# Kernel optimization log

Measured on AMD Instinct MI355X. Metric: run time of the kernel, lower is better.

## Reference

```python
import jax, jax.numpy as jnp
import numpy as np

EMBED = 384; HEADS = 12; POINTS = 9; LAYERS = 2
KFG = 20; KBG = 50; NITER = 10
B = 4; H = 64; W = 64


def _layer_norm(x, g, b, eps=1e-5):
    m = x.mean(-1, keepdims=True)
    v = ((x - m) ** 2).mean(-1, keepdims=True)
    return (x - m) * jax.lax.rsqrt(v + eps) * g + b


def _sine_pos(pad, C):
    # pad [B,H,W], 1.0 = padded. SinePositionalEncoding(num_feats=C//2, normalize=True)
    nf = C // 2
    not_m = 1.0 - pad
    y = jnp.cumsum(not_m, axis=1)
    x = jnp.cumsum(not_m, axis=2)
    eps = 1e-6; sc = 2.0 * np.pi
    y = y / (y[:, -1:, :] + eps) * sc
    x = x / (x[:, :, -1:] + eps) * sc
    t = jnp.arange(nf, dtype=jnp.float32)
    dim_t = 10000.0 ** (2.0 * jnp.floor(t / 2.0) / nf)
    px = x[..., None] / dim_t
    py = y[..., None] / dim_t
    def inter(p):
        b_, h_, w_, _ = p.shape
        return jnp.stack((jnp.sin(p[..., 0::2]), jnp.cos(p[..., 1::2])), -1).reshape(b_, h_, w_, nf)
    pos = jnp.concatenate([inter(py), inter(px)], -1)  # [B,H,W,C]
    return pos.reshape(pad.shape[0], -1, C)


def _kmeans(x, w, K, n_iter):
    # masked Lloyd k-means. x [B,N,C], w [B,N] in {0,1} (1 = member of the group)
    Bq, N, C = x.shape
    score = w - (jnp.arange(N, dtype=x.dtype) / N) * 1e-3  # earliest in-group points first
    _, idx = jax.lax.top_k(score, K)
    centers = jnp.take_along_axis(x, idx[:, :, None], axis=1)  # [B,K,C]
    xsq = jnp.sum(x * x, -1)
    def body(i, c):
        d = xsq[:, :, None] - 2.0 * jnp.einsum('bnc,bkc->bnk', x, c) + jnp.sum(c * c, -1)[:, None, :]
        a = jax.nn.one_hot(jnp.argmin(d, -1), K, dtype=x.dtype) * w[:, :, None]
        num = jnp.einsum('bnk,bnc->bkc', a, x)
        den = jnp.sum(a, 1)[:, :, None]
        return jnp.where(den > 0, num / jnp.maximum(den, 1e-6), c)
    return jax.lax.fori_loop(0, n_iter, body, centers)


def _bilinear(value, loc, Hs, Ws):
    # value [B,heads,HW,hd]; loc [B,N,heads,P,2] normalized (x,y); zero padding outside
    Bq, nh, HW, hd = value.shape
    x = loc[..., 0] * Ws - 0.5
    y = loc[..., 1] * Hs - 0.5
    x0 = jnp.floor(x); y0 = jnp.floor(y)
    def tr(t):
        return jnp.transpose(t, (0, 2, 1, 3)).reshape(Bq, nh, -1)  # -> [B,heads,N*P]
    wx = tr(x - x0)[..., None]
    wy = tr(y - y0)[..., None]
    x0i = x0.astype(jnp.int32); y0i = y0.astype(jnp.int32)
    def gather(xi, yi):
        valid = (xi >= 0) & (xi < Ws) & (yi >= 0) & (yi < Hs)
        idx = jnp.clip(yi, 0, Hs - 1) * Ws + jnp.clip(xi, 0, Ws - 1)
        g = jnp.take_along_axis(value, tr(idx)[..., None], axis=2)  # [B,heads,N*P,hd]
        return g * tr(valid.astype(value.dtype))[..., None]
    v00 = gather(x0i, y0i)
    v01 = gather(x0i + 1, y0i)
    v10 = gather(x0i, y0i + 1)
    v11 = gather(x0i + 1, y0i + 1)
    out = v00 * (1 - wx) * (1 - wy) + v01 * wx * (1 - wy) + v10 * (1 - wx) * wy + v11 * wx * wy
    return out.reshape(Bq, nh, -1, POINTS, hd)  # [B,heads,N,P,hd]


def _forward(s_x, s_padding_mask, supp_mask, Wv, bv, Woff, boff, Wa, ba, Wout, bout,
             ln1_g, ln1_b, Wf1, Wf2, ln2_g, ln2_b):
    Bq, C, Hs, Ws = s_x.shape
    N = Hs * Ws
    hd = C // HEADS
    pad = (s_padding_mask[:, 0] == 255.0).astype(s_x.dtype)  # 1 = padded
    obj = (supp_mask[:, 0] == 1.0).astype(s_x.dtype)
    x = s_x.reshape(Bq, C, N).transpose(0, 2, 1)  # [B,N,C]
    padf = pad.reshape(Bq, N)
    objf = obj.reshape(Bq, N)
    # FG/BG k-means clustering of valid pixels (Cluster tool, n_iter=10)
    fg_c = _kmeans(x, objf * (1.0 - padf), KFG, NITER)
    bg_c = _kmeans(x, (1.0 - objf) * (1.0 - padf), KBG, NITER)
    pos = _sine_pos(pad, C)
    ry, rx = jnp.meshgrid(jnp.linspace(0.5, Hs - 0.5, Hs) / Hs,
                          jnp.linspace(0.5, Ws - 0.5, Ws) / Ws, indexing='ij')
    ref = jnp.stack([rx.reshape(-1), ry.reshape(-1)], -1)[None]  # [1,N,2] (x,y)
    wh = jnp.array([Ws, Hs], dtype=s_x.dtype)
    for l in range(LAYERS):
        q = x + pos
        v = (x * (1.0 - padf)[..., None]) @ Wv[l] + bv[l]
        v = v.reshape(Bq, N, HEADS, hd).transpose(0, 2, 1, 3)  # [B,heads,N,hd]
        off = (q @ Woff[l] + boff[l]).reshape(Bq, N, HEADS, POINTS, 2)
        aw = jax.nn.softmax((q @ Wa[l] + ba[l]).reshape(Bq, N, HEADS, POINTS), axis=-1)
        loc = ref[:, :, None, None, :] + off / wh
        samp = _bilinear(v, loc, Hs, Ws)  # [B,heads,N,P,hd]
        attn = jnp.einsum('bhnpd,bnhp->bnhd', samp, aw).reshape(Bq, N, C)
        x = _layer_norm(x + attn @ Wout[l] + bout[l], ln1_g[l], ln1_b[l])
        x = _layer_norm(x + jax.nn.relu(x @ Wf1[l]) @ Wf2[l], ln2_g[l], ln2_b[l])
    return jnp.concatenate([x, fg_c, bg_c], axis=1)  # [B, N+70, C]


def setup_inputs():
    key = jax.random.key(0)
    ks = jax.random.split(key, 12)
    dt = jnp.float32
    s = 0.02
    p = lambda k, shp: jax.random.normal(k, shp, dt) * s
    s_x = jax.random.normal(ks[0], (B, EMBED, H, W), dt)
    pad = jnp.zeros((B, 1, H, W), dt).at[:, :, :, W - 8:].set(255.0)  # right border padded
    supp_mask = (jax.random.uniform(ks[1], (B, 1, H, W)) < 0.15).astype(dt)
    return dict(
        s_x=s_x, s_padding_mask=pad, supp_mask=supp_mask,
        Wv=p(ks[2], (LAYERS, EMBED, EMBED)), bv=jnp.zeros((LAYERS, EMBED), dt),
        Woff=p(ks[3], (LAYERS, EMBED, HEADS * POINTS * 2)), boff=p(ks[4], (LAYERS, HEADS * POINTS * 2)),
        Wa=p(ks[5], (LAYERS, EMBED, HEADS * POINTS)), ba=jnp.zeros((LAYERS, HEADS * POINTS), dt),
        Wout=p(ks[6], (LAYERS, EMBED, EMBED)), bout=jnp.zeros((LAYERS, EMBED), dt),
        ln1_g=jnp.ones((LAYERS, EMBED), dt), ln1_b=jnp.zeros((LAYERS, EMBED), dt),
        Wf1=p(ks[7], (LAYERS, EMBED, 3 * EMBED)), Wf2=p(ks[8], (LAYERS, 3 * EMBED, EMBED)),
        ln2_g=jnp.ones((LAYERS, EMBED), dt), ln2_b=jnp.zeros((LAYERS, EMBED), dt))


def reference(s_x, s_padding_mask, supp_mask, Wv, bv, Woff, boff, Wa, ba, Wout, bout,
              ln1_g, ln1_b, Wf1, Wf2, ln2_g, ln2_b):
    return _forward(s_x, s_padding_mask, supp_mask, Wv, bv, Woff, boff, Wa, ba, Wout, bout,
                    ln1_g, ln1_b, Wf1, Wf2, ln2_g, ln2_b)
```

## Files before the change

kernel.cpp:

```cpp
#include <hip/hip_runtime.h>
#include <hip/hip_bf16.h>
#include <math.h>

#define NB 4
#define CE 384
#define NH 12
#define DH 32
#define NPTS 9
#define NLAYERS 2
#define KFG 20
#define KBG 50
#define NITER 10
#define HDIM 64
#define WDIM 64
#define NPIX 4096
#define BNTOT (NB * NPIX)
#define NROW (NPIX + KFG + KBG)
#define TWO_PI 6.283185307179586f

#define AS1 __attribute__((address_space(1)))
#define AS3 __attribute__((address_space(3)))

typedef __attribute__((ext_vector_type(8))) short short8;
typedef __attribute__((ext_vector_type(4))) float float4v;

static __device__ __forceinline__ unsigned short f2bf(float f) {
  __hip_bfloat16 h = __float2bfloat16(f);
  return *reinterpret_cast<unsigned short*>(&h);
}
static __device__ __forceinline__ float bf2f(unsigned short u) {
  unsigned x = ((unsigned)u) << 16;
  return __uint_as_float(x);
}

__device__ __forceinline__ float4 sample4(const float* __restrict__ vb, int xi, int yi, int c) {
  bool valid = (xi >= 0) & (xi < WDIM) & (yi >= 0) & (yi < HDIM);
  int xc = min(max(xi, 0), WDIM - 1), yc = min(max(yi, 0), HDIM - 1);
  float4 g = *(const float4*)(vb + (long)(yc * WDIM + xc) * CE + c);
  if (!valid) { g.x = 0.f; g.y = 0.f; g.z = 0.f; g.w = 0.f; }
  return g;
}

__global__ void k_masks(const float* __restrict__ pm, const float* __restrict__ sm,
                        float* padf, float* objf, float* notp, float* wfg, float* wbg) {
  int i = blockIdx.x * 256 + threadIdx.x;
  if (i >= NB * NPIX) return;
  float p  = (pm[i] == 255.0f) ? 1.f : 0.f;
  float o  = (sm[i] == 1.0f) ? 1.f : 0.f;
  float np_ = 1.f - p;
  padf[i] = p; objf[i] = o; notp[i] = np_;
  wfg[i] = o * np_;
  wbg[i] = (1.f - o) * np_;
}

__global__ __launch_bounds__(256) void k_transpose(const float* __restrict__ sx,
                                                   float* __restrict__ X) {
  __shared__ float tile[64][65];
  int nb = blockIdx.x * 64, cb = blockIdx.y * 64, b = blockIdx.z;
  int t = threadIdx.x;
  for (int idx = t; idx < 64 * 64; idx += 256) {
    int cc = idx >> 6, nn = idx & 63;
    tile[cc][nn] = sx[((long)b * CE + cb + cc) * NPIX + nb + nn];
  }
  __syncthreads();
  for (int idx = t; idx < 64 * 64; idx += 256) {
    int nn = idx >> 6, cc = idx & 63;
    X[((long)b * NPIX + nb + nn) * CE + cb + cc] = tile[cc][nn];
  }
}

__global__ void k_xsq(const float* __restrict__ X, double* __restrict__ xsq) {
  int row = blockIdx.x; int t = threadIdx.x;
  const float* xr = X + (long)row * CE;
  double s = 0.0;
  for (int i = t; i < CE; i += 64) { double v = (double)xr[i]; s += v * v; }
  #pragma unroll
  for (int o = 32; o > 0; o >>= 1) s += __shfl_down(s, o, 64);
  if (t == 0) xsq[row] = s;
}

__global__ __launch_bounds__(128) void k_cums(const float* __restrict__ padf,
                                              float* __restrict__ yvf,
                                              float* __restrict__ xvf,
                                              float* __restrict__ invdt) {
  __shared__ float pad_s[NPIX];
  int b = blockIdx.x; int t = threadIdx.x;
  for (int i = t; i < NPIX; i += 128) pad_s[i] = padf[b * NPIX + i];
  if (b == 0) {
    for (int c = t; c < CE; c += 128) {
      int tt = (c < 192) ? c : c - 192;
      invdt[c] = 1.0f / powf(10000.0f, (float)(2 * (tt / 2)) / 192.0f);
    }
  }
  __syncthreads();
  if (t < 64) {
    int w = t;
    float cum[64]; float tot = 0.f;
    for (int h = 0; h < 64; ++h) {
      float nm = 1.f - pad_s[h * WDIM + w];
      tot += nm; cum[h] = tot;
    }
    float sc = 1.f / (tot + 1e-6f);
    for (int h = 0; h < 64; ++h) yvf[b * NPIX + h * WDIM + w] = cum[h] * sc * TWO_PI;
  } else {
    int h = t - 64;
    float cum[64]; float tot = 0.f;
    for (int w = 0; w < 64; ++w) {
      float nm = 1.f - pad_s[h * WDIM + w];
      tot += nm; cum[w] = tot;
    }
    float sc = 1.f / (tot + 1e-6f);
    for (int w = 0; w < 64; ++w) xvf[b * NPIX + h * WDIM + w] = cum[w] * sc * TWO_PI;
  }
}

__global__ void k_kinit(const float* __restrict__ X, const float* __restrict__ wts,
                        float* __restrict__ cen, int K) {
  int b = blockIdx.x;
  __shared__ int idx[KBG];
  if (threadIdx.x == 0) {
    int cnt = 0;
    for (int n = 0; n < NPIX && cnt < K; ++n) if (wts[b * NPIX + n] > 0.f) idx[cnt++] = n;
    for (int n = 0; n < NPIX && cnt < K; ++n) if (!(wts[b * NPIX + n] > 0.f)) idx[cnt++] = n;
  }
  __syncthreads();
  for (int i = threadIdx.x; i < K * CE; i += blockDim.x) {
    int k = i / CE, c = i % CE;
    cen[((long)b * K + k) * CE + c] = X[((long)b * NPIX + idx[k]) * CE + c];
  }
}

#define HSTR4 104
#define KSTR4 416

__global__ __launch_bounds__(256) void k_dots(
    const float* __restrict__ X, const double* __restrict__ xsq,
    const float* __restrict__ cenF, const float* __restrict__ cenB,
    float* __restrict__ candD, int* __restrict__ candI, int* __restrict__ cntAll) {
  __shared__ float ct[10 * KSTR4];
  __shared__ float csq_s[10];
  int z = blockIdx.y;
  int isBg = (z >= 2) ? 1 : 0;
  int k0 = isBg ? (z - 2) * 10 : z * 10;
  int t = threadIdx.x;
  int h = t & 3;
  int n = blockIdx.x * 128 + (t >> 2) * 2;
  int b = blockIdx.x >> 5;
  if (blockIdx.x == 0 && z == 0) {
    for (int i = t; i < NB * (KFG + KBG); i += 256) cntAll[i] = 0;
  }
  const float* cb = (isBg ? cenB + (long)b * KBG * CE
                          : cenF + (long)b * KFG * CE) + (long)k0 * CE;
  for (int i = t; i < 10 * CE; i += 256) {
    int k = i / CE, c = i % CE;
    ct[k * KSTR4 + (c / 96) * HSTR4 + (c % 96)] = cb[i];
  }
  {
    int w = t >> 6, lane = t & 63;
    for (int kk = w; kk < 10; kk += 4) {
      double s = 0.0;
      for (int c = lane; c < CE; c += 64) { double v = (double)cb[kk * CE + c]; s += v * v; }
      #pragma unroll
      for (int o = 32; o > 0; o >>= 1) s += __shfl_down(s, o, 64);
      if (lane == 0) csq_s[kk] = (float)s;
    }
  }
  __syncthreads();
  const float* xr = X + (long)n * CE + h * 96;
  const float* cth = ct + h * HSTR4;
  float acc[10][2];
  #pragma unroll
  for (int k = 0; k < 10; ++k) { acc[k][0] = 0.f; acc[k][1] = 0.f; }
  for (int c0 = 0; c0 < 96; c0 += 8) {
    float4 xa[2], xb[2];
    #pragma unroll
    for (int p = 0; p < 2; ++p) {
      xa[p] = *(const float4*)(xr + p * CE + c0);
      xb[p] = *(const float4*)(xr + p * CE + c0 + 4);
    }
    #pragma unroll
    for (int k = 0; k < 10; ++k) {
      float4 c1 = *(const float4*)(&cth[k * KSTR4 + c0]);
      float4 c2 = *(const float4*)(&cth[k * KSTR4 + c0 + 4]);
      #pragma unroll
      for (int p = 0; p < 2; ++p) {
        float a = acc[k][p];
        a += xa[p].x * c1.x; a += xa[p].y * c1.y;
        a += xa[p].z * c1.z; a += xa[p].w * c1.w;
        a += xb[p].x * c2.x; a += xb[p].y * c2.y;
        a += xb[p].z * c2.z; a += xb[p].w * c2.w;
        acc[k][p] = a;
      }
    }
  }
  #pragma unroll
  for (int k = 0; k < 10; ++k)
    #pragma unroll
    for (int p = 0; p < 2; ++p) {
      float a = acc[k][p];
      a += __shfl_xor(a, 1, 64);
      a += __shfl_xor(a, 2, 64);
      acc[k][p] = a;
    }
  if (h == 0) {
    #pragma unroll
    for (int p = 0; p < 2; ++p) {
      float qn = (float)xsq[n + p];
      float best = 3.0e38f; int bi = 0;
      #pragma unroll
      for (int k = 0; k < 10; ++k) {
        float d = qn - 2.0f * acc[k][p] + csq_s[k];
        if (d < best) { best = d; bi = k0 + k; }
      }
      long gi = (long)z * BNTOT + n + p;
      candD[gi] = best;
      candI[gi] = bi;
    }
  }
}

__global__ void k_asn(const float* __restrict__ candD, const int* __restrict__ candI,
                      const float* __restrict__ wfg, const float* __restrict__ wbg,
                      int* __restrict__ listF, int* __restrict__ listB,
                      int* __restrict__ cntAll) {
  int n = blockIdx.x * 256 + threadIdx.x;
  if (n >= BNTOT) return;
  int b = n >> 12;
  int nn = n & (NPIX - 1);
  float wf = wfg[n], wb = wbg[n];
  if (wf > 0.f) {
    float d0 = candD[n]; int i0 = candI[n];
    float d1 = candD[(long)BNTOT + n];
    if (d1 < d0) { d0 = d1; i0 = candI[(long)BNTOT + n]; }
    int slot = atomicAdd(&cntAll[b * KFG + i0], 1);
    listF[((long)b * KFG + i0) * NPIX + slot] = nn;
  } else if (wb > 0.f) {
    float d0 = candD[2L * BNTOT + n]; int i0 = candI[2L * BNTOT + n];
    #pragma unroll
    for (int z = 3; z < 7; ++z) {
      float dz = candD[(long)z * BNTOT + n];
      if (dz < d0) { d0 = dz; i0 = candI[(long)z * BNTOT + n]; }
    }
    int slot = atomicAdd(&cntAll[NB * KFG + b * KBG + i0], 1);
    listB[((long)b * KBG + i0) * NPIX + slot] = nn;
  }
}

__global__ __launch_bounds__(128) void k_cacc(
    const float* __restrict__ X,
    const int* __restrict__ listF, const int* __restrict__ listB,
    const int* __restrict__ cntAll,
    const float* __restrict__ srcF, float* __restrict__ dstF,
    const float* __restrict__ srcB, float* __restrict__ dstB) {
  __shared__ int ls[NPIX];
  int slice = blockIdx.x;
  int kq = blockIdx.y;
  int b = blockIdx.z;
  int t = threadIdx.x;
  int c = slice * 128 + t;
  const int* list; int cnt; const float* src; float* dst; long o;
  if (kq < KFG) {
    cnt = cntAll[b * KFG + kq];
    list = listF + ((long)b * KFG + kq) * NPIX;
    o = ((long)b * KFG + kq) * CE + c;
    src = srcF; dst = dstF;
  } else {
    int k = kq - KFG;
    cnt = cntAll[NB * KFG + b * KBG + k];
    list = listB + ((long)b * KBG + k) * NPIX;
    o = ((long)b * KBG + k) * CE + c;
    src = srcB; dst = dstB;
  }
  for (int i = t; i < cnt; i += 128) ls[i] = list[i];
  __syncthreads();
  const float* Xb = X + (long)b * NPIX * CE;
  double acc = 0.0;
  int i = 0;
  for (; i + 4 <= cnt; i += 4) {
    int n0 = ls[i], n1 = ls[i + 1], n2 = ls[i + 2], n3 = ls[i + 3];
    float v0 = Xb[(long)n0 * CE + c];
    float v1 = Xb[(long)n1 * CE + c];
    float v2 = Xb[(long)n2 * CE + c];
    float v3 = Xb[(long)n3 * CE + c];
    acc += (double)v0; acc += (double)v1; acc += (double)v2; acc += (double)v3;
  }
  for (; i < cnt; ++i) acc += (double)Xb[(long)ls[i] * CE + c];
  dst[o] = (cnt > 0) ? (float)(acc / (double)cnt) : src[o];
}

__global__ void k_cvtQV(const float* __restrict__ X,
                        const float* __restrict__ yvf, const float* __restrict__ xvf,
                        const float* __restrict__ invdt, const float* __restrict__ notp,
                        float* __restrict__ POS,
                        unsigned short* __restrict__ QB, unsigned short* __restrict__ VBin) {
  long i = (long)blockIdx.x * 256 + threadIdx.x;
  if (i >= (long)NB * NPIX * CE) return;
  int c = (int)(i % CE);
  long row = i / CE;
  float p = (c < 192) ? yvf[row] : xvf[row];
  float v = p * invdt[c];
  int tt = (c < 192) ? c : c - 192;
  float r = (tt & 1) ? cosf(v) : sinf(v);
  POS[i] = r;
  float x = X[i];
  QB[i] = f2bf(x + r);
  VBin[i] = f2bf(x * notp[row]);
}

__global__ void k_cvtW_all(
    const float* __restrict__ Wv_l, const float* __restrict__ Woff_l,
    const float* __restrict__ Wa_l, const float* __restrict__ Wout_l,
    const float* __restrict__ Wf1_l, const float* __restrict__ Wf2_l,
    const float* __restrict__ boff_l, const float* __restrict__ ba_l,
    unsigned short* __restrict__ W0, unsigned short* __restrict__ W1,
    unsigned short* __restrict__ W3, unsigned short* __restrict__ W4,
    unsigned short* __restrict__ W5, float* __restrict__ biasCat) {
  int i = blockIdx.x * 256 + threadIdx.x;
  const int S = 147456, SF = 442368;
  if (i < S) {
    int n = i / 384, k = i % 384;
    W0[i] = f2bf(Wv_l[(long)k * 384 + n]);
  } else if (i < 2 * S) {
    int j = i - S; int n = j / 384, k = j % 384;
    float v = 0.f;
    if (n < 216) v = Woff_l[(long)k * 216 + n];
    else if (n < 324) v = Wa_l[(long)k * 108 + (n - 216)];
    W1[j] = f2bf(v);
  } else if (i < 3 * S) {
    int j = i - 2 * S; int n = j / 384, k = j % 384;
    W3[j] = f2bf(Wout_l[(long)k * 384 + n]);
  } else if (i < 3 * S + SF) {
    int j = i - 3 * S; int n = j / 384, k = j % 384;
    W4[j] = f2bf(Wf1_l[(long)k * 1152 + n]);
  } else if (i < 3 * S + 2 * SF) {
    int j = i - 3 * S - SF; int n = j / 1152, k = j % 1152;
    W5[j] = f2bf(Wf2_l[(long)k * 384 + n]);
  } else if (i < 3 * S + 2 * SF + 324) {
    int j = i - 3 * S - 2 * SF;
    biasCat[j] = (j < 216) ? boff_l[j] : ba_l[j - 216];
  }
}

__global__ __launch_bounds__(256) void k_gemm_bf(
    const unsigned short* __restrict__ A, const unsigned short* __restrict__ Bt,
    const float* __restrict__ bias, float* __restrict__ Cf, unsigned short* __restrict__ Cb,
    int M, int K, int N, int relu) {
  __shared__ unsigned short As[128 * 32];
  __shared__ unsigned short Bs[128 * 32];
  int bx, by;
  {
    int gx = gridDim.x;
    int q = blockIdx.y * gx + blockIdx.x;
    if ((gridDim.y & 7) == 0) {
      int xcd = q & 7;
      int r = q >> 3;
      bx = r % gx;
      by = xcd + 8 * (r / gx);
    } else { bx = blockIdx.x; by = blockIdx.y; }
  }
  int m0 = by * 128, n0 = bx * 128;
  int t = threadIdx.x;
  int w = t >> 6, l = t & 63;
  int wm = w >> 1, wn = w & 1;
  int half = l >> 4, lr = l & 15;
  float4v acc[4][4] = {};
  for (int k0 = 0; k0 < K; k0 += 32) {
    #pragma unroll
    for (int i = 0; i < 2; ++i) {
      int c = w * 64 + i * 256 + l;
      int r = c >> 2, part = c & 3;
      int ldsOff = (w * 64 + i * 256) * 8;
      __builtin_amdgcn_global_load_lds(
          (const AS1 unsigned int*)(A + (size_t)(m0 + r) * K + k0 + part * 8),
          (AS3 unsigned int*)(As + ldsOff), 16, 0, 0);
      __builtin_amdgcn_global_load_lds(
          (const AS1 unsigned int*)(Bt + (size_t)(n0 + r) * K + k0 + part * 8),
          (AS3 unsigned int*)(Bs + ldsOff), 16, 0, 0);
    }
    __syncthreads();
    short8 af[4], bfr[4];
    #pragma unroll
    for (int am = 0; am < 4; ++am)
      af[am] = *(const short8*)(&As[(wm * 64 + am * 16 + lr) * 32 + half * 8]);
    #pragma unroll
    for (int bn = 0; bn < 4; ++bn)
      bfr[bn] = *(const short8*)(&Bs[(wn * 64 + bn * 16 + lr) * 32 + half * 8]);
    #pragma unroll
    for (int am = 0; am < 4; ++am)
      #pragma unroll
      for (int bn = 0; bn < 4; ++bn)
        acc[am][bn] = __builtin_amdgcn_mfma_f32_16x16x32_bf16(af[am], bfr[bn], acc[am][bn], 0, 0, 0);
    __syncthreads();
  }
  #pragma unroll
  for (int am = 0; am < 4; ++am) {
    #pragma unroll
    for (int bn = 0; bn < 4; ++bn) {
      int gc = n0 + wn * 64 + bn * 16 + lr;
      if (gc < N) {
        float bv = bias ? bias[gc] : 0.f;
        int gr0 = m0 + wm * 64 + am * 16 + half * 4;
        #pragma unroll
        for (int r = 0; r < 4; ++r) {
          float v = acc[am][bn][r] + bv;
          if (relu) v = fmaxf(v, 0.f);
          size_t oi = (size_t)(gr0 + r) * N + gc;
          if (Cf) Cf[oi] = v;
          else Cb[oi] = f2bf(v);
        }
      }
    }
  }
}

__global__ void k_coords(const unsigned short* __restrict__ OAB, float4* __restrict__ CRD) {
  int idx = blockIdx.x * 256 + threadIdx.x;
  if (idx >= NB * NPIX * NH) return;
  int row = idx / NH, h = idx % NH;
  int n = row & (NPIX - 1);
  int hh = n >> 6, ww = n & 63;
  float refx = ((float)ww + 0.5f) / (float)WDIM;
  float refy = ((float)hh + 0.5f) / (float)HDIM;
  const unsigned short* oab = OAB + (size_t)row * 324;
  float f[NPTS];
  #pragma unroll
  for (int j = 0; j < NPTS; ++j) f[j] = bf2f(oab[216 + h * 9 + j]);
  float m = f[0];
  #pragma unroll
  for (int j = 1; j < NPTS; ++j) m = fmaxf(m, f[j]);
  float s = 0.f;
  #pragma unroll
  for (int j = 0; j < NPTS; ++j) { f[j] = expf(f[j] - m); s += f[j]; }
  float inv = 1.f / s;
  float4* crd = CRD + (size_t)row * 108 + h * 9;
  #pragma unroll
  for (int p = 0; p < NPTS; ++p) {
    float ox = bf2f(oab[h * 18 + p * 2 + 0]);
    float oy = bf2f(oab[h * 18 + p * 2 + 1]);
    float lx = refx + ox / (float)WDIM;
    float ly = refy + oy / (float)HDIM;
    float xs = lx * (float)WDIM - 0.5f;
    float ys = ly * (float)HDIM - 0.5f;
    float x0f = floorf(xs), y0f = floorf(ys);
    int x0 = (int)x0f, y0 = (int)y0f;
    float4 o;
    o.x = xs - x0f;
    o.y = ys - y0f;
    o.z = f[p] * inv;
    o.w = __int_as_float((y0 << 16) | (x0 & 0xFFFF));
    crd[p] = o;
  }
}

__global__ __launch_bounds__(256) void k_gather(
    const float* __restrict__ V, const float4* __restrict__ CRD,
    uint2* __restrict__ ATTu) {
  int idx = blockIdx.x * 256 + threadIdx.x;
  if (idx >= NB * NPIX * (CE / 4)) return;
  int row = idx / (CE / 4), cq = idx % (CE / 4);
  int c = cq * 4;
  int h = c >> 5;
  int b = row >> 12;
  const float* vb = V + (size_t)b * NPIX * CE;
  const float4* crd = CRD + (size_t)row * 108 + h * 9;
  float a0 = 0.f, a1 = 0.f, a2 = 0.f, a3 = 0.f;
  #pragma unroll
  for (int p = 0; p < NPTS; ++p) {
    float4 o = crd[p];
    int pk = __float_as_int(o.w);
    int x0 = (int)(short)(pk & 0xFFFF);
    int y0 = pk >> 16;
    float wx = o.x, wy = o.y, aw = o.z;
    float4 g00 = sample4(vb, x0,     y0,     c);
    float4 g01 = sample4(vb, x0 + 1, y0,     c);
    float4 g10 = sample4(vb, x0,     y0 + 1, c);
    float4 g11 = sample4(vb, x0 + 1, y0 + 1, c);
    float w00 = (1.f - wx) * (1.f - wy), w01 = wx * (1.f - wy);
    float w10 = (1.f - wx) * wy,         w11 = wx * wy;
    a0 += aw * (g00.x * w00 + g01.x * w01 + g10.x * w10 + g11.x * w11);
    a1 += aw * (g00.y * w00 + g01.y * w01 + g10.y * w10 + g11.y * w11);
    a2 += aw * (g00.z * w00 + g01.z * w01 + g10.z * w10 + g11.z * w11);
    a3 += aw * (g00.w * w00 + g01.w * w01 + g10.w * w10 + g11.w * w11);
  }
  uint2 pk2;
  pk2.x = (unsigned)f2bf(a0) | ((unsigned)f2bf(a1) << 16);
  pk2.y = (unsigned)f2bf(a2) | ((unsigned)f2bf(a3) << 16);
  ATTu[(size_t)row * (CE / 4) + cq] = pk2;
}

__global__ __launch_bounds__(256) void k_ln(
    float* __restrict__ X, const float* __restrict__ T,
    const float* __restrict__ g, const float* __restrict__ bb,
    unsigned short* __restrict__ xbOut,
    const float* __restrict__ posp, const float* __restrict__ notp,
    unsigned short* __restrict__ qb, unsigned short* __restrict__ vbin,
    float* __restrict__ outp) {
  int t = threadIdx.x;
  int row = blockIdx.x * 4 + (t >> 6);
  int lane = t & 63;
  float* xr = X + (long)row * CE;
  const float* tr = T + (long)row * CE;
  float v[6]; float s = 0.f;
  #pragma unroll
  for (int i = 0; i < 6; ++i) { v[i] = xr[lane + 64 * i] + tr[lane + 64 * i]; s += v[i]; }
  #pragma unroll
  for (int o = 32; o > 0; o >>= 1) s += __shfl_down(s, o, 64);
  s = __shfl(s, 0, 64);
  float m = s / (float)CE;
  float var = 0.f;
  #pragma unroll
  for (int i = 0; i < 6; ++i) { float d = v[i] - m; var += d * d; }
  #pragma unroll
  for (int o = 32; o > 0; o >>= 1) var += __shfl_down(var, o, 64);
  var = __shfl(var, 0, 64);
  float rst = rsqrtf(var / (float)CE + 1e-5f);
  float nprow = notp ? notp[row] : 0.f;
  int b = row >> 12, n = row & (NPIX - 1);
  #pragma unroll
  for (int i = 0; i < 6; ++i) {
    int c = lane + 64 * i;
    float xn = (v[i] - m) * rst * g[c] + bb[c];
    if (outp) outp[((long)b * NROW + n) * CE + c] = xn;
    else xr[c] = xn;
    if (xbOut) xbOut[(long)row * CE + c] = f2bf(xn);
    if (qb) {
      qb[(long)row * CE + c] = f2bf(xn + posp[(long)row * CE + c]);
      vbin[(long)row * CE + c] = f2bf(xn * nprow);
    }
  }
}

__global__ void k_out_cen(const float* __restrict__ fg, const float* __restrict__ bg,
                          float* __restrict__ out) {
  int i = blockIdx.x * 256 + threadIdx.x;
  const int tot = NB * (KFG + KBG) * CE;
  if (i >= tot) return;
  int c = i % CE;
  int r = i / CE;
  int rr = r % (KFG + KBG);
  int b = r / (KFG + KBG);
  float v;
  if (rr < KFG) v = fg[((long)b * KFG + rr) * CE + c];
  else v = bg[((long)b * KBG + (rr - KFG)) * CE + c];
  out[((long)b * NROW + NPIX + rr) * CE + c] = v;
}

extern "C" void kernel_launch(void* const* d_in, const int* in_sizes, int n_in,
                              void* d_out, int out_size, void* d_ws, size_t ws_size,
                              hipStream_t stream) {
  (void)in_sizes; (void)n_in; (void)out_size; (void)ws_size;
  const float* s_x  = (const float*)d_in[0];
  const float* s_pm = (const float*)d_in[1];
  const float* s_sm = (const float*)d_in[2];
  const float* Wv   = (const float*)d_in[3];
  const float* bv   = (const float*)d_in[4];
  const float* Woff = (const float*)d_in[5];
  const float* boff = (const float*)d_in[6];
  const float* Wa   = (const float*)d_in[7];
  const float* ba   = (const float*)d_in[8];
  const float* Wout = (const float*)d_in[9];
  const float* bout = (const float*)d_in[10];
  const float* ln1g = (const float*)d_in[11];
  const float* ln1b = (const float*)d_in[12];
  const float* Wf1  = (const float*)d_in[13];
  const float* Wf2  = (const float*)d_in[14];
  const float* ln2g = (const float*)d_in[15];
  const float* ln2b = (const float*)d_in[16];
  float* out = (float*)d_out;
  char* pb = (char*)d_ws;

  const long BN  = (long)NB * NPIX;
  const long BNC = BN * CE;

  float* X    = (float*)pb; pb += BNC * 4;
  float* POS  = (float*)pb; pb += BNC * 4;
  float* V    = (float*)pb; pb += BNC * 4;
  float* T2   = (float*)pb; pb += BNC * 4;
  unsigned short* QB   = (unsigned short*)pb; pb += BNC * 2;
  unsigned short* VBin = (unsigned short*)pb; pb += BNC * 2;
  unsigned short* T1b  = (unsigned short*)pb; pb += BNC * 2;
  unsigned short* Zbf  = QB;
  unsigned short* XB   = (unsigned short*)pb; pb += BNC * 2;
  unsigned short* OAB  = (unsigned short*)pb; pb += BN * 324 * 2;
  float4* CRD = (float4*)pb; pb += BN * 108 * 16;
  const int S_W = 147456, S_F = 442368;
  unsigned short* WT[NLAYERS][5];
  float* biasCat[NLAYERS];
  for (int l = 0; l < NLAYERS; ++l) {
    WT[l][0] = (unsigned short*)pb; pb += S_W * 2;
    WT[l][1] = (unsigned short*)pb; pb += S_W * 2;
    WT[l][2] = (unsigned short*)pb; pb += S_W * 2;
    WT[l][3] = (unsigned short*)pb; pb += S_F * 2;
    WT[l][4] = (unsigned short*)pb; pb += S_F * 2;
    biasCat[l] = (float*)pb; pb += 324 * 4;
  }
  float* padf = (float*)pb; pb += BN * 4;
  float* objf = (float*)pb; pb += BN * 4;
  float* notp = (float*)pb; pb += BN * 4;
  float* wfg  = (float*)pb; pb += BN * 4;
  float* wbg  = (float*)pb; pb += BN * 4;
  float* yvf  = (float*)pb; pb += BN * 4;
  float* xvf  = (float*)pb; pb += BN * 4;
  float* invdt = (float*)pb; pb += CE * 4;
  pb = (char*)(((size_t)pb + 7) & ~(size_t)7);
  double* xsq   = (double*)pb; pb += BN * 8;
  float* candD = (float*)pb; pb += BN * 7 * 4;
  float* cFgA = (float*)pb; pb += (long)NB * KFG * CE * 4;
  float* cFgB = (float*)pb; pb += (long)NB * KFG * CE * 4;
  float* cBgA = (float*)pb; pb += (long)NB * KBG * CE * 4;
  float* cBgB = (float*)pb; pb += (long)NB * KBG * CE * 4;
  int* candI  = (int*)pb; pb += BN * 7 * 4;
  int* cntAll = (int*)pb; pb += NB * (KFG + KBG) * 4;
  int* listF  = (int*)pb; pb += (long)NB * KFG * NPIX * 4;
  int* listB  = (int*)pb; pb += (long)NB * KBG * NPIX * 4;

  int bn = (int)BN;
  int cvtBlocks = (int)((BNC + 255) / 256);

  k_masks<<<(bn + 255) / 256, 256, 0, stream>>>(s_pm, s_sm, padf, objf, notp, wfg, wbg);
  k_transpose<<<dim3(NPIX / 64, CE / 64, NB), 256, 0, stream>>>(s_x, X);
  k_xsq<<<bn, 64, 0, stream>>>(X, xsq);
  k_cums<<<NB, 128, 0, stream>>>(padf, yvf, xvf, invdt);
  k_cvtQV<<<cvtBlocks, 256, 0, stream>>>(X, yvf, xvf, invdt, notp, POS, QB, VBin);

  const int CVTW_TOT = 3 * S_W + 2 * S_F + 324;
  for (int l = 0; l < NLAYERS; ++l) {
    k_cvtW_all<<<(CVTW_TOT + 255) / 256, 256, 0, stream>>>(
        Wv + (long)l * CE * CE, Woff + (long)l * CE * 216, Wa + (long)l * CE * 108,
        Wout + (long)l * CE * CE, Wf1 + (long)l * CE * 1152, Wf2 + (long)l * 1152 * CE,
        boff + l * 216, ba + l * 108,
        WT[l][0], WT[l][1], WT[l][2], WT[l][3], WT[l][4], biasCat[l]);
  }

  float *srcF = cFgA, *dstF = cFgB, *srcB = cBgA, *dstB = cBgB;
  k_kinit<<<NB, 256, 0, stream>>>(X, wfg, srcF, KFG);
  k_kinit<<<NB, 256, 0, stream>>>(X, wbg, srcB, KBG);
  for (int it = 0; it < NITER; ++it) {
    k_dots<<<dim3(bn / 128, 7), 256, 0, stream>>>(X, xsq, srcF, srcB, candD, candI, cntAll);
    k_asn<<<(bn + 255) / 256, 256, 0, stream>>>(candD, candI, wfg, wbg, listF, listB, cntAll);
    k_cacc<<<dim3(3, KFG + KBG, NB), 128, 0, stream>>>(
        X, listF, listB, cntAll, srcF, dstF, srcB, dstB);
    float* tmp;
    tmp = srcF; srcF = dstF; dstF = tmp;
    tmp = srcB; srcB = dstB; dstB = tmp;
  }
  float* fgC = srcF; float* bgC = srcB;

  for (int l = 0; l < NLAYERS; ++l) {
    const float* bv_l   = bv   + l * CE;
    const float* bout_l = bout + l * CE;
    int last = (l == NLAYERS - 1);

    k_gemm_bf<<<dim3(3, 128), 256, 0, stream>>>(VBin, WT[l][0], bv_l, V, (unsigned short*)nullptr,
                                                bn, CE, 384, 0);
    k_gemm_bf<<<dim3(3, 128), 256, 0, stream>>>(QB, WT[l][1], biasCat[l], (float*)nullptr, OAB,
                                                bn, CE, 324, 0);
    k_coords<<<(bn * NH + 255) / 256, 256, 0, stream>>>(OAB, CRD);
    k_gather<<<(bn * (CE / 4) + 255) / 256, 256, 0, stream>>>(V, CRD, (uint2*)T1b);
    k_gemm_bf<<<dim3(3, 128), 256, 0, stream>>>(T1b, WT[l][2], bout_l, T2, (unsigned short*)nullptr,
                                                bn, CE, 384, 0);
    k_ln<<<bn / 4, 256, 0, stream>>>(X, T2, ln1g + l * CE, ln1b + l * CE,
                                     XB, (const float*)nullptr, (const float*)nullptr,
                                     (unsigned short*)nullptr, (unsigned short*)nullptr,
                                     (float*)nullptr);
    k_gemm_bf<<<dim3(9, 128), 256, 0, stream>>>(XB, WT[l][3], (const float*)nullptr,
                                                (float*)nullptr, Zbf, bn, CE, 1152, 1);
    k_gemm_bf<<<dim3(3, 128), 256, 0, stream>>>(Zbf, WT[l][4], (const float*)nullptr,
                                                T2, (unsigned short*)nullptr, bn, 1152, 384, 0);
    if (!last) {
      k_ln<<<bn / 4, 256, 0, stream>>>(X, T2, ln2g + l * CE, ln2b + l * CE,
                                       (unsigned short*)nullptr, POS, notp, QB, VBin,
                                       (float*)nullptr);
    } else {
      k_ln<<<bn / 4, 256, 0, stream>>>(X, T2, ln2g + l * CE, ln2b + l * CE,
                                       (unsigned short*)nullptr, (const float*)nullptr,
                                       (const float*)nullptr, (unsigned short*)nullptr,
                                       (unsigned short*)nullptr, out);
    }
  }

  k_out_cen<<<(NB * (KFG + KBG) * CE + 255) / 256, 256, 0, stream>>>(fgC, bgC, out);
}
```

Measured before the change: 1.416 ms.

## Split k-means centroid accumulation into chunks with separate reduction kernel

Each cluster's member list is now split into 16 chunks. Each chunk is summed by its own block into a double-precision partial buffer, which reuses the V workspace. A new reduction kernel then adds the partials and divides by the count to produce the new centers. This targets long serial gather loops and load imbalance when some clusters hold thousands of points, at the cost of an extra launch and partial-sum traffic per iteration.

```diff
diff --git a/kernel.cpp b/kernel.cpp
--- a/kernel.cpp
+++ b/kernel.cpp
@@ -16,6 +16,7 @@
 #define NPIX 4096
 #define BNTOT (NB * NPIX)
 #define NROW (NPIX + KFG + KBG)
+#define NCH 16
 #define TWO_PI 6.283185307179586f
 
 #define AS1 __attribute__((address_space(1)))
@@ -250,33 +251,33 @@
     const float* __restrict__ X,
     const int* __restrict__ listF, const int* __restrict__ listB,
     const int* __restrict__ cntAll,
-    const float* __restrict__ srcF, float* __restrict__ dstF,
-    const float* __restrict__ srcB, float* __restrict__ dstB) {
-  __shared__ int ls[NPIX];
+    double* __restrict__ PC) {
+  __shared__ int ls[256];
   int slice = blockIdx.x;
   int kq = blockIdx.y;
-  int b = blockIdx.z;
+  int zz = blockIdx.z;
+  int b = zz / NCH, ch = zz % NCH;
   int t = threadIdx.x;
   int c = slice * 128 + t;
-  const int* list; int cnt; const float* src; float* dst; long o;
+  const int* list; int cnt;
   if (kq < KFG) {
     cnt = cntAll[b * KFG + kq];
     list = listF + ((long)b * KFG + kq) * NPIX;
-    o = ((long)b * KFG + kq) * CE + c;
-    src = srcF; dst = dstF;
   } else {
     int k = kq - KFG;
     cnt = cntAll[NB * KFG + b * KBG + k];
     list = listB + ((long)b * KBG + k) * NPIX;
-    o = ((long)b * KBG + k) * CE + c;
-    src = srcB; dst = dstB;
-  }
-  for (int i = t; i < cnt; i += 128) ls[i] = list[i];
+  }
+  int cs = (cnt + NCH - 1) / NCH;
+  int i0 = ch * cs;
+  int i1 = min(i0 + cs, cnt);
+  int m = i1 - i0;
+  for (int i = t; i < m; i += 128) ls[i] = list[i0 + i];
   __syncthreads();
   const float* Xb = X + (long)b * NPIX * CE;
   double acc = 0.0;
   int i = 0;
-  for (; i + 4 <= cnt; i += 4) {
+  for (; i + 4 <= m; i += 4) {
     int n0 = ls[i], n1 = ls[i + 1], n2 = ls[i + 2], n3 = ls[i + 3];
     float v0 = Xb[(long)n0 * CE + c];
     float v1 = Xb[(long)n1 * CE + c];
@@ -284,8 +285,34 @@
     float v3 = Xb[(long)n3 * CE + c];
     acc += (double)v0; acc += (double)v1; acc += (double)v2; acc += (double)v3;
   }
-  for (; i < cnt; ++i) acc += (double)Xb[(long)ls[i] * CE + c];
-  dst[o] = (cnt > 0) ? (float)(acc / (double)cnt) : src[o];
+  for (; i < m; ++i) acc += (double)Xb[(long)ls[i] * CE + c];
+  PC[((long)ch * (NB * (KFG + KBG)) + (long)b * (KFG + KBG) + kq) * CE + c] = acc;
+}
+
+__global__ void k_cred(const double* __restrict__ PC, const int* __restrict__ cntAll,
+                       const float* __restrict__ srcF, float* __restrict__ dstF,
+                       const float* __restrict__ srcB, float* __restrict__ dstB) {
+  int i = blockIdx.x * 256 + threadIdx.x;
+  const int tot = NB * (KFG + KBG) * CE;
+  if (i >= tot) return;
+  int c = i % CE;
+  int r = i / CE;
+  int kq = r % (KFG + KBG);
+  int b = r / (KFG + KBG);
+  const long stride = (long)NB * (KFG + KBG) * CE;
+  double s = 0.0;
+  #pragma unroll
+  for (int ch = 0; ch < NCH; ++ch) s += PC[(long)ch * stride + (long)r * CE + c];
+  if (kq < KFG) {
+    int cnt = cntAll[b * KFG + kq];
+    long o = ((long)b * KFG + kq) * CE + c;
+    dstF[o] = (cnt > 0) ? (float)(s / (double)cnt) : srcF[o];
+  } else {
+    int k = kq - KFG;
+    int cnt = cntAll[NB * KFG + b * KBG + k];
+    long o = ((long)b * KBG + k) * CE + c;
+    dstB[o] = (cnt > 0) ? (float)(s / (double)cnt) : srcB[o];
+  }
 }
 
 __global__ void k_cvtQV(const float* __restrict__ X,
@@ -576,6 +603,7 @@
   float* POS  = (float*)pb; pb += BNC * 4;
   float* V    = (float*)pb; pb += BNC * 4;
   float* T2   = (float*)pb; pb += BNC * 4;
+  double* PC  = (double*)V;
   unsigned short* QB   = (unsigned short*)pb; pb += BNC * 2;
   unsigned short* VBin = (unsigned short*)pb; pb += BNC * 2;
   unsigned short* T1b  = (unsigned short*)pb; pb += BNC * 2;
@@ -635,11 +663,13 @@
   float *srcF = cFgA, *dstF = cFgB, *srcB = cBgA, *dstB = cBgB;
   k_kinit<<<NB, 256, 0, stream>>>(X, wfg, srcF, KFG);
   k_kinit<<<NB, 256, 0, stream>>>(X, wbg, srcB, KBG);
+  const int credBlocks = (NB * (KFG + KBG) * CE + 255) / 256;
   for (int it = 0; it < NITER; ++it) {
     k_dots<<<dim3(bn / 128, 7), 256, 0, stream>>>(X, xsq, srcF, srcB, candD, candI, cntAll);
     k_asn<<<(bn + 255) / 256, 256, 0, stream>>>(candD, candI, wfg, wbg, listF, listB, cntAll);
-    k_cacc<<<dim3(3, KFG + KBG, NB), 128, 0, stream>>>(
-        X, listF, listB, cntAll, srcF, dstF, srcB, dstB);
+    k_cacc<<<dim3(3, KFG + KBG, NB * NCH), 128, 0, stream>>>(
+        X, listF, listB, cntAll, PC);
+    k_cred<<<credBlocks, 256, 0, stream>>>(PC, cntAll, srcF, dstF, srcB, dstB);
     float* tmp;
     tmp = srcF; srcF = dstF; dstF = tmp;
     tmp = srcB; srcB = dstB; dstB = tmp;
```

New measurement: 1.299 ms. -8.3%, faster.
